# Performance work log

Hardware: AMD Instinct MI355X
Metric: run time of the kernel (lower is better)

Reference implementation:

```python
import jax, jax.numpy as jnp
import numpy as np

N_OPS = 32
D_REASON = 128
TOP_K = 2
EPS = 1e-05
LEAK = 1e-05  # coefficient on the all-ops leak term


def setup_inputs() -> dict:
    key = jax.random.key(0)
    k1, k2, k3, k4 = jax.random.split(key, 4)
    B, S = 8, 2048
    x = jax.random.normal(k1, (B, S, D_REASON), dtype=jnp.float32)
    indices = jax.random.randint(k2, (B, S, TOP_K), 0, N_OPS, dtype=jnp.int64)
    weights = jax.random.uniform(k3, (B, S, TOP_K), dtype=jnp.float32)
    ops = 0.02 * jax.random.normal(k4, (N_OPS, D_REASON, D_REASON), dtype=jnp.float32)
    return {"x": x, "indices": indices, "weights": weights, "ops": ops}


def _ternary_effective(ops):
    # scale_n = clamp(mean|W_n|, 1e-5); q = STE ternary quantize; W_eff = q * scale
    scale = jnp.maximum(jnp.mean(jnp.abs(ops), axis=(1, 2)), EPS)  # (N,)
    q_hard = jnp.clip(jnp.round(ops / scale[:, None, None]), -1.0, 1.0)
    # STE: identity gradient w.r.t. ops through the quantizer
    q = ops + jax.lax.stop_gradient(q_hard - ops)
    return q * scale[:, None, None]  # (N, D, D)


def reference(x, indices, weights, ops):
    # x: (B,S,D); indices: (B,S,K) int; weights: (B,S,K); ops: (N,D,D)
    w_eff = _ternary_effective(ops)  # (N, D_out, D_in)
    # F.linear(x, W) = x @ W.T, for every op at once -> T: (B,S,N,D_out)
    T = jnp.einsum("bsd,nod->bsno", x, w_eff)
    total = T.sum(axis=2)  # sum over all ops, (B,S,D)
    # gather the selected top_k ops per token: (B,S,K,D)
    gathered = jnp.take_along_axis(T, indices[..., None].astype(jnp.int32), axis=2)
    routed = jnp.sum(weights[..., None] * gathered, axis=2)  # (B,S,D)
    return LEAK * total / N_OPS + routed
```

## Files before the change

### kernel.cpp

```cpp
#include <hip/hip_runtime.h>

#define N_OPS 32
#define D 128
#define MAT (D * D)
#define EPS 1e-5f
#define NTOK (8 * 2048)
#define NASSIGN (NTOK * 2)
#define CAP 34816
#define NSEG (CAP / 64)

typedef __attribute__((ext_vector_type(8))) short short8;
typedef __attribute__((ext_vector_type(4))) float f32x4;

__device__ inline unsigned short f2bf(float f) {
    unsigned int u = __float_as_uint(f);
    return (unsigned short)((u + 0x7FFF + ((u >> 16) & 1)) >> 16);
}
__device__ inline float bf2f(unsigned int h) {
    return __uint_as_float(h << 16);
}

__global__ __launch_bounds__(256) void k_prep(const float* __restrict__ ops,
                                              const int* __restrict__ idx,
                                              float* __restrict__ scale,
                                              int* __restrict__ list,
                                              unsigned short* __restrict__ wb) {
    const int b = blockIdx.x;
    const int tid = threadIdx.x;
    if (b < N_OPS) {
        const int e = b;
        const float* W = ops + e * MAT;
        float s = 0.f;
        for (int i = tid; i < MAT; i += 256) s += fabsf(W[i]);
        for (int off = 32; off; off >>= 1) s += __shfl_xor(s, off);
        __shared__ float red[4];
        __shared__ float s_scale;
        const int lane = tid & 63, wid = tid >> 6;
        if (lane == 0) red[wid] = s;
        __syncthreads();
        if (tid == 0) {
            s_scale = fmaxf((red[0] + red[1] + red[2] + red[3]) / (float)MAT, EPS);
            scale[e] = s_scale;
        }
        __syncthreads();
        const float sc = s_scale;
#pragma unroll
        for (int it = 0; it < 8; ++it) {
            const int f = it * 256 + tid;
            const int o = f >> 4, dc = f & 15;
            const float4* wp = (const float4*)(W + o * D + dc * 8);
            float4 a = wp[0], c = wp[1];
            float v[8] = {a.x, a.y, a.z, a.w, c.x, c.y, c.z, c.w};
            unsigned short q[8];
#pragma unroll
            for (int j = 0; j < 8; ++j) {
                float t = rintf(v[j] / sc);
                t = fminf(1.f, fmaxf(-1.f, t));
                q[j] = (t == 0.f) ? 0 : (t > 0.f ? 0x3F80 : 0xBF80);
            }
            ((short8*)wb)[e * 2048 + dc * 128 + o] = *(const short8*)q;
        }
    } else {
        const int cb = b - 32;
        __shared__ int hl[1024];
        __shared__ int stot[N_OPS], soff[N_OPS + 1], sbase[N_OPS], lh[N_OPS];
        for (int i = tid; i < 1024; i += 256) hl[i] = 0;
        if (tid < N_OPS) lh[tid] = 0;
        __syncthreads();
#pragma unroll 4
        for (int j = 0; j < 32; ++j) {
            const int4 e4 = ((const int4*)idx)[j * 256 + tid];
            atomicAdd(&hl[(j << 5) | e4.x], 1);
            atomicAdd(&hl[(j << 5) | e4.y], 1);
            atomicAdd(&hl[(j << 5) | e4.z], 1);
            atomicAdd(&hl[(j << 5) | e4.w], 1);
        }
        __syncthreads();
        if (tid < N_OPS) {
            int t = 0;
            for (int c = 0; c < 32; ++c) t += hl[c * N_OPS + tid];
            stot[tid] = t;
        }
        __syncthreads();
        if (tid == 0) {
            int run = 0;
            for (int e = 0; e < N_OPS; ++e) { soff[e] = run; run += (stot[e] + 63) & ~63; }
            soff[N_OPS] = run;
        }
        __syncthreads();
        if (tid < N_OPS) {
            int r = soff[tid];
            for (int c = 0; c < cb; ++c) r += hl[c * N_OPS + tid];
            sbase[tid] = r;
        }
        __syncthreads();
#pragma unroll
        for (int j = 0; j < 4; ++j) {
            const int a = cb * 1024 + j * 256 + tid;
            const int e = idx[a];
            const int r = atomicAdd(&lh[e], 1);
            list[sbase[e] + r] = (e << 20) | a;
        }
        for (int s = soff[cb] + stot[cb] + tid; s < soff[cb + 1]; s += 256)
            list[s] = -1;
        if (cb == 0)
            for (int s = soff[N_OPS] + tid; s < CAP; s += 256) list[s] = -1;
    }
}

__global__ __launch_bounds__(256, 4) void k_mfma(const float* __restrict__ x,
                                                 const int* __restrict__ list,
                                                 const unsigned short* __restrict__ wb,
                                                 const float* __restrict__ scale,
                                                 const float* __restrict__ wts,
                                                 unsigned short* __restrict__ partial) {
    const int lane = threadIdx.x & 63;
    const int wv   = threadIdx.x >> 6;
    const int quad = lane >> 4;
    const int ncol = lane & 15;

    const int base = blockIdx.x * 64;
    const int v0 = list[base];
    if (v0 < 0) return;
    const int e = v0 >> 20;
    const float sc = scale[e];
    const short8* src = (const short8*)wb + e * 2048;

    const int rowbase = base + wv * 16;
    const int v = list[rowbase + ncol];
    const int tok = (v < 0) ? 0 : ((v & 0xFFFFF) >> 1);
    const float4* Axp = (const float4*)(x + (size_t)tok * D);
    float4 Ar[8];
#pragma unroll
    for (int s = 0; s < 4; ++s) {
        Ar[2 * s]     = Axp[s * 8 + quad * 2];
        Ar[2 * s + 1] = Axp[s * 8 + quad * 2 + 1];
    }

    f32x4 acc[8];
#pragma unroll
    for (int j = 0; j < 8; ++j) acc[j] = (f32x4){0.f, 0.f, 0.f, 0.f};
#pragma unroll
    for (int s = 0; s < 4; ++s) {
        const float4 f0 = Ar[2 * s], f1 = Ar[2 * s + 1];
        const unsigned short a8[8] = {f2bf(f0.x), f2bf(f0.y), f2bf(f0.z), f2bf(f0.w),
                                      f2bf(f1.x), f2bf(f1.y), f2bf(f1.z), f2bf(f1.w)};
        const short8 a = *(const short8*)a8;
        const short8* Bp = src + (s * 4 + quad) * 128;
#pragma unroll
        for (int nt = 0; nt < 8; ++nt) {
            const short8 bb = Bp[nt * 16 + ncol];
            acc[nt] = __builtin_amdgcn_mfma_f32_16x16x32_bf16(a, bb, acc[nt], 0, 0, 0);
        }
    }
#pragma unroll
    for (int r = 0; r < 4; ++r) {
        const int vr = __shfl(v, quad * 4 + r);
        if (vr < 0) continue;
        const int ar = vr & 0xFFFFF;
        const float wsc = wts[ar] * sc;
        unsigned short* pp = partial + (size_t)ar * D;
#pragma unroll
        for (int nt = 0; nt < 8; ++nt)
            pp[nt * 16 + ncol] = f2bf(wsc * acc[nt][r]);
    }
}

__global__ __launch_bounds__(256) void k_final(const unsigned short* __restrict__ partial,
                                               float* __restrict__ out) {
    const int i = blockIdx.x * 256 + threadIdx.x;
    const int t = i >> 5, c = i & 31;
    const uint2 p0 = ((const uint2*)(partial + (size_t)(2 * t) * D))[c];
    const uint2 p1 = ((const uint2*)(partial + (size_t)(2 * t + 1) * D))[c];
    float4 o;
    o.x = bf2f(p0.x & 0xFFFFu) + bf2f(p1.x & 0xFFFFu);
    o.y = bf2f(p0.x >> 16)     + bf2f(p1.x >> 16);
    o.z = bf2f(p0.y & 0xFFFFu) + bf2f(p1.y & 0xFFFFu);
    o.w = bf2f(p0.y >> 16)     + bf2f(p1.y >> 16);
    ((float4*)out)[i] = o;
}

extern "C" void kernel_launch(void* const* d_in, const int* in_sizes, int n_in,
                              void* d_out, int out_size, void* d_ws, size_t ws_size,
                              hipStream_t stream) {
    const float* x   = (const float*)d_in[0];
    const int*   idx = (const int*)  d_in[1];
    const float* wts = (const float*)d_in[2];
    const float* ops = (const float*)d_in[3];
    float* out = (float*)d_out;

    unsigned short* wb      = (unsigned short*)d_ws;
    unsigned short* partial = wb + (size_t)N_OPS * MAT;
    float*          scale   = (float*)(partial + (size_t)NASSIGN * D);
    int*            list    = (int*)(scale + 32);

    k_prep<<<64, 256, 0, stream>>>(ops, idx, scale, list, wb);
    k_mfma<<<NSEG, 256, 0, stream>>>(x, list, wb, scale, wts, partial);
    k_final<<<NTOK * D / 4 / 256, 256, 0, stream>>>(partial, out);
}
```

Baseline: 97.58 us.

## Fuse weight quantization and routing into per-(op,chunk) GEMM blocks with LDS weights

Merges the prep and MFMA kernels into one. Each block handles one op and one chunk of assignments: it recomputes the ternary scale, quantizes the op's weights into LDS, and builds its row list with a block-wide prefix scan. It then runs MFMA tiles that read the weights from LDS instead of global memory. This drops a kernel launch and the global list/weight round trip, but every op's weights are now reduced and quantized 32 times, and the final kernel becomes a grid-stride loop.

```diff
diff --git a/kernel.cpp b/kernel.cpp
--- a/kernel.cpp
+++ b/kernel.cpp
@@ -6,8 +6,8 @@
 #define EPS 1e-5f
 #define NTOK (8 * 2048)
 #define NASSIGN (NTOK * 2)
-#define CAP 34816
-#define NSEG (CAP / 64)
+#define NCHUNK 32
+#define CHUNK (NASSIGN / NCHUNK)
 
 typedef __attribute__((ext_vector_type(8))) short short8;
 typedef __attribute__((ext_vector_type(4))) float f32x4;
@@ -20,164 +20,130 @@
     return __uint_as_float(h << 16);
 }
 
-__global__ __launch_bounds__(256) void k_prep(const float* __restrict__ ops,
+__global__ __launch_bounds__(256) void k_gemm(const float* __restrict__ ops,
                                               const int* __restrict__ idx,
-                                              float* __restrict__ scale,
-                                              int* __restrict__ list,
-                                              unsigned short* __restrict__ wb) {
-    const int b = blockIdx.x;
+                                              const float* __restrict__ x,
+                                              const float* __restrict__ wts,
+                                              unsigned short* __restrict__ partial) {
+    __shared__ short8 lB[2048];
+    __shared__ float red[4];
+    __shared__ float s_scale;
+    __shared__ int scn[256];
+    __shared__ int rows[192];
+
+    const int e   = blockIdx.x >> 5;
+    const int c   = blockIdx.x & 31;
     const int tid = threadIdx.x;
-    if (b < N_OPS) {
-        const int e = b;
-        const float* W = ops + e * MAT;
-        float s = 0.f;
-        for (int i = tid; i < MAT; i += 256) s += fabsf(W[i]);
-        for (int off = 32; off; off >>= 1) s += __shfl_xor(s, off);
-        __shared__ float red[4];
-        __shared__ float s_scale;
-        const int lane = tid & 63, wid = tid >> 6;
-        if (lane == 0) red[wid] = s;
+    const int lane = tid & 63;
+    const int wid  = tid >> 6;
+
+    const int4 v4 = ((const int4*)idx)[c * (CHUNK / 4) + tid];
+
+    const float* W = ops + e * MAT;
+    float s = 0.f;
+    for (int i = tid; i < MAT; i += 256) s += fabsf(W[i]);
+    for (int off = 32; off; off >>= 1) s += __shfl_xor(s, off);
+    if (lane == 0) red[wid] = s;
+    __syncthreads();
+    if (tid == 0)
+        s_scale = fmaxf((red[0] + red[1] + red[2] + red[3]) / (float)MAT, EPS);
+    __syncthreads();
+    const float sc = s_scale;
+
+#pragma unroll
+    for (int it = 0; it < 8; ++it) {
+        const int f = it * 256 + tid;
+        const int o = f >> 4, dc = f & 15;
+        const float4* wp = (const float4*)(W + o * D + dc * 8);
+        const float4 a = wp[0], b = wp[1];
+        const float v[8] = {a.x, a.y, a.z, a.w, b.x, b.y, b.z, b.w};
+        unsigned short q[8];
+#pragma unroll
+        for (int j = 0; j < 8; ++j) {
+            float t = rintf(v[j] / sc);
+            t = fminf(1.f, fmaxf(-1.f, t));
+            q[j] = (t == 0.f) ? 0 : (t > 0.f ? 0x3F80 : 0xBF80);
+        }
+        lB[dc * 128 + o] = *(const short8*)q;
+    }
+
+    const int cnt = (v4.x == e) + (v4.y == e) + (v4.z == e) + (v4.w == e);
+    scn[tid] = cnt;
+    __syncthreads();
+    for (int d = 1; d < 256; d <<= 1) {
+        const int v = scn[tid];
+        const int add = (tid >= d) ? scn[tid - d] : 0;
         __syncthreads();
-        if (tid == 0) {
-            s_scale = fmaxf((red[0] + red[1] + red[2] + red[3]) / (float)MAT, EPS);
-            scale[e] = s_scale;
-        }
+        scn[tid] = v + add;
         __syncthreads();
-        const float sc = s_scale;
-#pragma unroll
-        for (int it = 0; it < 8; ++it) {
-            const int f = it * 256 + tid;
-            const int o = f >> 4, dc = f & 15;
-            const float4* wp = (const float4*)(W + o * D + dc * 8);
-            float4 a = wp[0], c = wp[1];
-            float v[8] = {a.x, a.y, a.z, a.w, c.x, c.y, c.z, c.w};
-            unsigned short q[8];
-#pragma unroll
-            for (int j = 0; j < 8; ++j) {
-                float t = rintf(v[j] / sc);
-                t = fminf(1.f, fmaxf(-1.f, t));
-                q[j] = (t == 0.f) ? 0 : (t > 0.f ? 0x3F80 : 0xBF80);
-            }
-            ((short8*)wb)[e * 2048 + dc * 128 + o] = *(const short8*)q;
-        }
-    } else {
-        const int cb = b - 32;
-        __shared__ int hl[1024];
-        __shared__ int stot[N_OPS], soff[N_OPS + 1], sbase[N_OPS], lh[N_OPS];
-        for (int i = tid; i < 1024; i += 256) hl[i] = 0;
-        if (tid < N_OPS) lh[tid] = 0;
-        __syncthreads();
-#pragma unroll 4
-        for (int j = 0; j < 32; ++j) {
-            const int4 e4 = ((const int4*)idx)[j * 256 + tid];
-            atomicAdd(&hl[(j << 5) | e4.x], 1);
-            atomicAdd(&hl[(j << 5) | e4.y], 1);
-            atomicAdd(&hl[(j << 5) | e4.z], 1);
-            atomicAdd(&hl[(j << 5) | e4.w], 1);
-        }
-        __syncthreads();
-        if (tid < N_OPS) {
-            int t = 0;
-            for (int c = 0; c < 32; ++c) t += hl[c * N_OPS + tid];
-            stot[tid] = t;
-        }
-        __syncthreads();
-        if (tid == 0) {
-            int run = 0;
-            for (int e = 0; e < N_OPS; ++e) { soff[e] = run; run += (stot[e] + 63) & ~63; }
-            soff[N_OPS] = run;
-        }
-        __syncthreads();
-        if (tid < N_OPS) {
-            int r = soff[tid];
-            for (int c = 0; c < cb; ++c) r += hl[c * N_OPS + tid];
-            sbase[tid] = r;
-        }
-        __syncthreads();
-#pragma unroll
-        for (int j = 0; j < 4; ++j) {
-            const int a = cb * 1024 + j * 256 + tid;
-            const int e = idx[a];
-            const int r = atomicAdd(&lh[e], 1);
-            list[sbase[e] + r] = (e << 20) | a;
-        }
-        for (int s = soff[cb] + stot[cb] + tid; s < soff[cb + 1]; s += 256)
-            list[s] = -1;
-        if (cb == 0)
-            for (int s = soff[N_OPS] + tid; s < CAP; s += 256) list[s] = -1;
     }
-}
+    int base = scn[tid] - cnt;
+    const int total = scn[255];
+    const int a0 = c * CHUNK + tid * 4;
+    if (v4.x == e) rows[base++] = a0;
+    if (v4.y == e) rows[base++] = a0 + 1;
+    if (v4.z == e) rows[base++] = a0 + 2;
+    if (v4.w == e) rows[base++] = a0 + 3;
+    for (int i = total + tid; i < ((total + 63) & ~63); i += 256) rows[i] = -1;
+    __syncthreads();
 
-__global__ __launch_bounds__(256, 4) void k_mfma(const float* __restrict__ x,
-                                                 const int* __restrict__ list,
-                                                 const unsigned short* __restrict__ wb,
-                                                 const float* __restrict__ scale,
-                                                 const float* __restrict__ wts,
-                                                 unsigned short* __restrict__ partial) {
-    const int lane = threadIdx.x & 63;
-    const int wv   = threadIdx.x >> 6;
     const int quad = lane >> 4;
     const int ncol = lane & 15;
+    const int wv   = wid;
 
-    const int base = blockIdx.x * 64;
-    const int v0 = list[base];
-    if (v0 < 0) return;
-    const int e = v0 >> 20;
-    const float sc = scale[e];
-    const short8* src = (const short8*)wb + e * 2048;
+    for (int g = 0; g < total; g += 64) {
+        const int v = rows[g + wv * 16 + ncol];
+        const int tok = (v < 0) ? 0 : (v >> 1);
+        const float4* Axp = (const float4*)(x + (size_t)tok * D);
+        float4 Ar[8];
+#pragma unroll
+        for (int ss = 0; ss < 4; ++ss) {
+            Ar[2 * ss]     = Axp[ss * 8 + quad * 2];
+            Ar[2 * ss + 1] = Axp[ss * 8 + quad * 2 + 1];
+        }
 
-    const int rowbase = base + wv * 16;
-    const int v = list[rowbase + ncol];
-    const int tok = (v < 0) ? 0 : ((v & 0xFFFFF) >> 1);
-    const float4* Axp = (const float4*)(x + (size_t)tok * D);
-    float4 Ar[8];
+        f32x4 acc[8];
 #pragma unroll
-    for (int s = 0; s < 4; ++s) {
-        Ar[2 * s]     = Axp[s * 8 + quad * 2];
-        Ar[2 * s + 1] = Axp[s * 8 + quad * 2 + 1];
-    }
-
-    f32x4 acc[8];
+        for (int j = 0; j < 8; ++j) acc[j] = (f32x4){0.f, 0.f, 0.f, 0.f};
 #pragma unroll
-    for (int j = 0; j < 8; ++j) acc[j] = (f32x4){0.f, 0.f, 0.f, 0.f};
+        for (int ss = 0; ss < 4; ++ss) {
+            const float4 f0 = Ar[2 * ss], f1 = Ar[2 * ss + 1];
+            const unsigned short a8[8] = {f2bf(f0.x), f2bf(f0.y), f2bf(f0.z), f2bf(f0.w),
+                                          f2bf(f1.x), f2bf(f1.y), f2bf(f1.z), f2bf(f1.w)};
+            const short8 a = *(const short8*)a8;
+            const short8* Bp = lB + (ss * 4 + quad) * 128;
 #pragma unroll
-    for (int s = 0; s < 4; ++s) {
-        const float4 f0 = Ar[2 * s], f1 = Ar[2 * s + 1];
-        const unsigned short a8[8] = {f2bf(f0.x), f2bf(f0.y), f2bf(f0.z), f2bf(f0.w),
-                                      f2bf(f1.x), f2bf(f1.y), f2bf(f1.z), f2bf(f1.w)};
-        const short8 a = *(const short8*)a8;
-        const short8* Bp = src + (s * 4 + quad) * 128;
+            for (int nt = 0; nt < 8; ++nt) {
+                const short8 bb = Bp[nt * 16 + ncol];
+                acc[nt] = __builtin_amdgcn_mfma_f32_16x16x32_bf16(a, bb, acc[nt], 0, 0, 0);
+            }
+        }
 #pragma unroll
-        for (int nt = 0; nt < 8; ++nt) {
-            const short8 bb = Bp[nt * 16 + ncol];
-            acc[nt] = __builtin_amdgcn_mfma_f32_16x16x32_bf16(a, bb, acc[nt], 0, 0, 0);
+        for (int r = 0; r < 4; ++r) {
+            const int vr = __shfl(v, quad * 4 + r);
+            if (vr < 0) continue;
+            const float wsc = wts[vr] * sc;
+            unsigned short* pp = partial + (size_t)vr * D;
+#pragma unroll
+            for (int nt = 0; nt < 8; ++nt)
+                pp[nt * 16 + ncol] = f2bf(wsc * acc[nt][r]);
         }
-    }
-#pragma unroll
-    for (int r = 0; r < 4; ++r) {
-        const int vr = __shfl(v, quad * 4 + r);
-        if (vr < 0) continue;
-        const int ar = vr & 0xFFFFF;
-        const float wsc = wts[ar] * sc;
-        unsigned short* pp = partial + (size_t)ar * D;
-#pragma unroll
-        for (int nt = 0; nt < 8; ++nt)
-            pp[nt * 16 + ncol] = f2bf(wsc * acc[nt][r]);
     }
 }
 
 __global__ __launch_bounds__(256) void k_final(const unsigned short* __restrict__ partial,
                                                float* __restrict__ out) {
-    const int i = blockIdx.x * 256 + threadIdx.x;
-    const int t = i >> 5, c = i & 31;
-    const uint2 p0 = ((const uint2*)(partial + (size_t)(2 * t) * D))[c];
-    const uint2 p1 = ((const uint2*)(partial + (size_t)(2 * t + 1) * D))[c];
-    float4 o;
-    o.x = bf2f(p0.x & 0xFFFFu) + bf2f(p1.x & 0xFFFFu);
-    o.y = bf2f(p0.x >> 16)     + bf2f(p1.x >> 16);
-    o.z = bf2f(p0.y & 0xFFFFu) + bf2f(p1.y & 0xFFFFu);
-    o.w = bf2f(p0.y >> 16)     + bf2f(p1.y >> 16);
-    ((float4*)out)[i] = o;
+    for (int i = blockIdx.x * 256 + threadIdx.x; i < NTOK * 32; i += 256 * 256) {
+        const int t = i >> 5, cc = i & 31;
+        const uint2 p0 = ((const uint2*)(partial + (size_t)(2 * t) * D))[cc];
+        const uint2 p1 = ((const uint2*)(partial + (size_t)(2 * t + 1) * D))[cc];
+        float4 o;
+        o.x = bf2f(p0.x & 0xFFFFu) + bf2f(p1.x & 0xFFFFu);
+        o.y = bf2f(p0.x >> 16)     + bf2f(p1.x >> 16);
+        o.z = bf2f(p0.y & 0xFFFFu) + bf2f(p1.y & 0xFFFFu);
+        o.w = bf2f(p0.y >> 16)     + bf2f(p1.y >> 16);
+        ((float4*)out)[i] = o;
+    }
 }
 
 extern "C" void kernel_launch(void* const* d_in, const int* in_sizes, int n_in,
@@ -189,12 +155,8 @@
     const float* ops = (const float*)d_in[3];
     float* out = (float*)d_out;
 
-    unsigned short* wb      = (unsigned short*)d_ws;
-    unsigned short* partial = wb + (size_t)N_OPS * MAT;
-    float*          scale   = (float*)(partial + (size_t)NASSIGN * D);
-    int*            list    = (int*)(scale + 32);
+    unsigned short* partial = (unsigned short*)d_ws;
 
-    k_prep<<<64, 256, 0, stream>>>(ops, idx, scale, list, wb);
-    k_mfma<<<NSEG, 256, 0, stream>>>(x, list, wb, scale, wts, partial);
-    k_final<<<NTOK * D / 4 / 256, 256, 0, stream>>>(partial, out);
+    k_gemm<<<N_OPS * NCHUNK, 256, 0, stream>>>(ops, idx, x, wts, partial);
+    k_final<<<256, 256, 0, stream>>>(partial, out);
 }
```

Result: slower. 116.6 us (+19.5%).
